# Kernel optimization log

Hardware: AMD Instinct MI355X
Metric: run time of the kernel (lower is better)

## Reference

```python
import jax, jax.numpy as jnp
import numpy as np

SIGMA = 1.5
KSIZE = 15

def _log_kernel(sigma=SIGMA, k=KSIZE):
    ax = np.arange(k, dtype=np.float32) - k // 2
    xx, yy, zz = np.meshgrid(ax, ax, ax, indexing='ij')
    rr2 = xx**2 + yy**2 + zz**2
    g = np.exp(-rr2 / (2.0 * sigma**2))
    g = g / g.sum()
    log = (rr2 - 3.0 * sigma**2) / sigma**4 * g
    log = log - log.mean()
    return jnp.asarray(log.reshape(1, 1, k, k, k), dtype=jnp.float32)  # OIDHW

_KERNEL = _log_kernel()
_PAD = KSIZE // 2

def setup_inputs() -> dict:
    key = jax.random.key(0)
    k1, k2 = jax.random.split(key)
    shape = (4, 160, 160, 160)
    pred = jax.random.normal(k1, shape, dtype=jnp.float32)
    target = jax.random.normal(k2, shape, dtype=jnp.float32)
    return {"pred": pred, "target": target}

def _conv_log(x):
    # x: [B, D, H, W] -> [B, 1, D, H, W] conv with LoG kernel, 'same' padding
    x = x[:, None]  # NCDHW
    return jax.lax.conv_general_dilated(
        x, _KERNEL.astype(x.dtype),
        window_strides=(1, 1, 1),
        padding=[(_PAD, _PAD)] * 3,
        dimension_numbers=('NCDHW', 'OIDHW', 'NCDHW'))

def reference(pred, target):
    fp = _conv_log(pred)
    ft = _conv_log(target)
    return jnp.mean(jnp.abs(fp - ft))
```

## Files before the change

### kernel.cpp

```cpp
#include <hip/hip_runtime.h>
#include <hip/hip_fp16.h>
#include <math.h>

#define KS   15
#define RAD  7
#define L    160
#define VOL  (L*L*L)
#define NB   4
#define WTL  32
#define HTL  80
#define HALO (HTL + 2*RAD)
#define LDA  34
#define RPT  5
#define DT   40
#define NBLK (5*10*16)

typedef float fx2 __attribute__((ext_vector_type(2)));
typedef float fx4 __attribute__((ext_vector_type(4)));

struct Taps {
    float g[KS];
    float h[KS];
    float m;
    float scale;
};

__device__ __forceinline__ fx4 ld4z(const float* __restrict__ p, int w) {
    if (w >= 0 && w + 3 < L) return *reinterpret_cast<const fx4*>(p + w);
    fx4 r;
    r.x = (w     >= 0 && w     < L) ? p[w]     : 0.f;
    r.y = (w + 1 >= 0 && w + 1 < L) ? p[w + 1] : 0.f;
    r.z = (w + 2 >= 0 && w + 2 < L) ? p[w + 2] : 0.f;
    r.w = (w + 3 >= 0 && w + 3 < L) ? p[w + 3] : 0.f;
    return r;
}

__global__ __launch_bounds__(256, 4) void k_wh(const float* __restrict__ pred,
                                               const float* __restrict__ tgt,
                                               __half2* __restrict__ PQ,
                                               __half* __restrict__ Rb,
                                               Taps tp) {
    __shared__ float   sA[HALO][LDA];
    __shared__ float   sB[HALO][LDA];
    __shared__ __half2 sC[HALO][LDA / 2];

    const int pflat = blockIdx.x + 10 * (blockIdx.y + 160 * blockIdx.z);
    const int wlog  = (pflat & 7) * 800 + (pflat >> 3);
    const int bxs   = wlog % 10;
    const int bys   = (wlog / 10) % 160;
    const int bzs   = wlog / 1600;

    const int tid = threadIdx.x;
    const int wt  = bxs >> 1;
    const int ht  = bxs & 1;
    const int wb  = wt * WTL;
    const int h0  = ht * HTL;
    const int d   = bys;
    const int n   = bzs;
    const size_t nbase = (size_t)n * VOL;
    const float* __restrict__ pro = pred + nbase + (size_t)d * L * L;
    const float* __restrict__ tro = tgt  + nbase + (size_t)d * L * L;
    const bool wedge = (wt == 0) || (wt == 4);

    for (int task = tid; task < HALO * 4; task += 256) {
        const int r  = task >> 2;
        const int j2 = task & 3;
        const int h  = h0 - RAD + r;
        if (h >= 0 && h < L) {
            const float* pr = pro + h * L;
            const float* tr = tro + h * L;
            const int w0 = wb + 8 * j2 - 8;
            float dv[24];
            if (!wedge) {
#pragma unroll
                for (int q = 0; q < 6; ++q) {
                    fx4 pv = *reinterpret_cast<const fx4*>(pr + w0 + 4 * q);
                    fx4 tv = *reinterpret_cast<const fx4*>(tr + w0 + 4 * q);
                    fx4 dd = pv - tv;
                    dv[4*q+0] = dd.x; dv[4*q+1] = dd.y;
                    dv[4*q+2] = dd.z; dv[4*q+3] = dd.w;
                }
            } else {
#pragma unroll
                for (int q = 0; q < 6; ++q) {
                    fx4 pv = ld4z(pr, w0 + 4 * q);
                    fx4 tv = ld4z(tr, w0 + 4 * q);
                    fx4 dd = pv - tv;
                    dv[4*q+0] = dd.x; dv[4*q+1] = dd.y;
                    dv[4*q+2] = dd.z; dv[4*q+3] = dd.w;
                }
            }
#pragma unroll
            for (int kp = 0; kp < 8; kp += 2) {
                fx2 mid = {dv[kp + 8], dv[kp + 9]};
                fx2 aa = tp.g[7] * mid;
                fx2 bb = tp.h[7] * mid;
                fx2 cc = mid;
#pragma unroll
                for (int u = 0; u < 7; ++u) {
                    fx2 sl = {dv[kp + 1 + u],  dv[kp + 2 + u]};
                    fx2 sr = {dv[kp + 15 - u], dv[kp + 16 - u]};
                    fx2 s  = sl + sr;
                    aa += tp.g[u] * s;
                    bb += tp.h[u] * s;
                    cc += s;
                }
                *reinterpret_cast<fx2*>(&sA[r][8*j2 + kp]) = aa;
                *reinterpret_cast<fx2*>(&sB[r][8*j2 + kp]) = bb;
                sC[r][(8*j2 + kp) >> 1] = __floats2half2_rn(cc.x, cc.y);
            }
        } else {
#pragma unroll
            for (int kp = 0; kp < 8; kp += 2) {
                fx2 z = {0.f, 0.f};
                *reinterpret_cast<fx2*>(&sA[r][8*j2 + kp]) = z;
                *reinterpret_cast<fx2*>(&sB[r][8*j2 + kp]) = z;
                sC[r][(8*j2 + kp) >> 1] = __floats2half2_rn(0.f, 0.f);
            }
        }
    }
    __syncthreads();

    {
        const int wg = tid & 15;
        const int ty = tid >> 4;
        fx2 p[RPT], q[RPT], rb[RPT];
#pragma unroll
        for (int k = 0; k < RPT; ++k) { p[k] = 0.f; q[k] = 0.f; rb[k] = 0.f; }
#pragma unroll
        for (int jr = 0; jr < RPT + 2 * RAD; ++jr) {
            const int srow = RPT * ty + jr;
            fx2 va = *reinterpret_cast<const fx2*>(&sA[srow][2*wg]);
            fx2 vb = *reinterpret_cast<const fx2*>(&sB[srow][2*wg]);
            float2 cf = __half22float2(sC[srow][wg]);
            fx2 vc = {cf.x, cf.y};
#pragma unroll
            for (int k = 0; k < RPT; ++k) {
                const int t = jr - k;
                if (t >= 0 && t < KS) {
                    p[k]  += tp.g[t] * va;
                    q[k]  += tp.h[t] * va + tp.g[t] * vb;
                    rb[k] += vc;
                }
            }
        }
#pragma unroll
        for (int k = 0; k < RPT; ++k) {
            const int h = h0 + RPT * ty + k;
            const size_t o = nbase + ((size_t)h * L + d) * L + wb + 2*wg;
            __half2 pq[2];
            pq[0] = __floats2half2_rn(p[k].x, q[k].x);
            pq[1] = __floats2half2_rn(p[k].y, q[k].y);
            *reinterpret_cast<int2*>(&PQ[o]) = *reinterpret_cast<int2*>(pq);
            __half2 rr = __floats2half2_rn(rb[k].x, rb[k].y);
            *reinterpret_cast<__half2*>(&Rb[o]) = rr;
        }
    }
}

__global__ __launch_bounds__(512) void k_d(const __half2* __restrict__ PQ,
                                           const __half* __restrict__ R,
                                           float* __restrict__ partial,
                                           Taps tp) {
    const int pflat = blockIdx.x + 5 * (blockIdx.y + 10 * blockIdx.z);
    const int wlog  = (pflat & 7) * 100 + (pflat >> 3);
    const int dc    = wlog & 3;
    const int rest  = wlog >> 2;
    const int bx    = rest % 5;
    const int by    = (rest / 5) % 10;
    const int n     = rest / 50;

    const int tx = threadIdx.x;
    const int ty = threadIdx.y;
    const int w  = bx * 32 + tx;
    const int h  = by * 16 + ty;
    const int d0 = dc * DT;

    const size_t base = (size_t)n * VOL + ((size_t)h * L) * L + w;
    const __half2* PQp = PQ + base;
    const __half*  Rp  = R  + base;

    float rp[KS], rq[KS], rc[KS];
    float box = 0.f;

#pragma unroll
    for (int i = 0; i < KS - 1; ++i) {
        int s = d0 - RAD + i;
        bool ok = (s >= 0);
        int off = s * L;
        float2 pq = make_float2(0.f, 0.f);
        float vc = 0.f;
        if (ok) {
            pq = __half22float2(PQp[off]);
            vc = __half2float(Rp[off]);
        }
        rp[i] = pq.x; rq[i] = pq.y; rc[i] = vc;
        box += vc;
    }

    float acc = 0.f;
#pragma unroll
    for (int k = 0; k < DT; ++k) {
        int s = d0 + RAD + k;
        bool ok = (s < L);
        int off = s * L;
        float2 pq = make_float2(0.f, 0.f);
        float vc = 0.f;
        if (ok) {
            pq = __half22float2(PQp[off]);
            vc = __half2float(Rp[off]);
        }
        const int ri = (KS - 1 + k) % KS;
        rp[ri] = pq.x; rq[ri] = pq.y; rc[ri] = vc;
        box += vc;

        float f = 0.f;
#pragma unroll
        for (int t = 0; t < KS; ++t) {
            const int ii = (k + t) % KS;
            f += tp.h[t] * rp[ii] + tp.g[t] * rq[ii];
        }
        f -= tp.m * box;
        acc += fabsf(f);

        box -= rc[k % KS];
    }
    acc *= tp.scale;

#pragma unroll
    for (int off = 32; off > 0; off >>= 1) acc += __shfl_down(acc, off);

    __shared__ float wsum[8];
    const int tid  = ty * 32 + tx;
    const int lane = tid & 63;
    const int wid  = tid >> 6;
    if (lane == 0) wsum[wid] = acc;
    __syncthreads();
    if (wid == 0) {
        float v = (lane < 8) ? wsum[lane] : 0.f;
#pragma unroll
        for (int off = 4; off > 0; off >>= 1) v += __shfl_down(v, off);
        if (lane == 0) {
            partial[wlog] = v;
        }
    }
}

__global__ __launch_bounds__(1024) void k_reduce(const float* __restrict__ partial,
                                                 float* __restrict__ out) {
    float v = 0.f;
    for (int i = threadIdx.x; i < NBLK; i += 1024) v += partial[i];
#pragma unroll
    for (int off = 32; off > 0; off >>= 1) v += __shfl_down(v, off);

    __shared__ float wsum[16];
    const int lane = threadIdx.x & 63;
    const int wid  = threadIdx.x >> 6;
    if (lane == 0) wsum[wid] = v;
    __syncthreads();
    if (wid == 0) {
        float s = (lane < 16) ? wsum[lane] : 0.f;
#pragma unroll
        for (int off = 8; off > 0; off >>= 1) s += __shfl_down(s, off);
        if (lane == 0) out[0] = s;
    }
}

extern "C" void kernel_launch(void* const* d_in, const int* in_sizes, int n_in,
                              void* d_out, int out_size, void* d_ws, size_t ws_size,
                              hipStream_t stream) {
    const float* pred = (const float*)d_in[0];
    const float* tgt  = (const float*)d_in[1];
    float* out = (float*)d_out;

    Taps tp;
    const double sigma = 1.5;
    double g1[KS], S = 0.0;
    for (int i = 0; i < KS; ++i) {
        double x = (double)(i - RAD);
        g1[i] = exp(-x * x / (2.0 * sigma * sigma));
        S += g1[i];
    }
    double sumH = 0.0;
    for (int i = 0; i < KS; ++i) {
        double x = (double)(i - RAD);
        double G = g1[i] / S;
        double H = (x * x - sigma * sigma) / (sigma * sigma * sigma * sigma) * G;
        tp.g[i] = (float)G;
        tp.h[i] = (float)H;
        sumH += H;
    }
    tp.m     = (float)(3.0 * sumH / (double)(KS * KS * KS));
    tp.scale = 1.0f / ((float)NB * (float)VOL);

    char* wsb = (char*)d_ws;
    __half2* PQ      = (__half2*)wsb;
    __half*  Rb      = (__half*)(wsb + (size_t)NB * VOL * 4);
    float*   partial = (float*)(wsb + (size_t)NB * VOL * 6);

    k_wh<<<dim3(10, L, NB), dim3(256), 0, stream>>>(pred, tgt, PQ, Rb, tp);
    k_d<<<dim3(5, 10, NB * 4), dim3(32, 16), 0, stream>>>(PQ, Rb, partial, tp);
    k_reduce<<<1, 1024, 0, stream>>>(partial, out);
}
```

Measured before the change: 113.3 us.

## Loop k_wh over depth chunks with double-buffered smem and register prefetch

Each k_wh block now handles 10 consecutive depth slices instead of one, ping-ponging two shared-memory buffers. The global loads for the next slice are issued into registers before the current slice's H-pass, and its W-pass runs afterwards, hiding load latency behind compute. Each of 188 threads now does a 16-wide W-conv instead of 8-wide, and zero halo rows are written once. The grid shrinks from 6400 to 640 blocks and occupancy hint drops to 2 per SIMD, which raises register pressure and reduces parallelism.

Result: slower. 149.0 us (+31.4%).

```diff
diff --git a/kernel.cpp b/kernel.cpp
--- a/kernel.cpp
+++ b/kernel.cpp
@@ -12,6 +12,8 @@
 #define HALO (HTL + 2*RAD)
 #define LDA  34
 #define RPT  5
+#define DCH  10
+#define NDC  16
 #define DT   40
 #define NBLK (5*10*16)
 
@@ -35,126 +37,168 @@
     return r;
 }
 
-__global__ __launch_bounds__(256, 4) void k_wh(const float* __restrict__ pred,
+__device__ __forceinline__ void wconv16(const float* dv, const Taps& tp,
+                                        float (*A)[LDA], float (*B)[LDA],
+                                        __half2 (*C)[LDA / 2], int r, int c0) {
+#pragma unroll
+    for (int kp = 0; kp < 16; kp += 2) {
+        fx2 mid = {dv[kp + 8], dv[kp + 9]};
+        fx2 aa = tp.g[7] * mid;
+        fx2 bb = tp.h[7] * mid;
+        fx2 cc = mid;
+#pragma unroll
+        for (int u = 0; u < 7; ++u) {
+            fx2 sl = {dv[kp + 1 + u],  dv[kp + 2 + u]};
+            fx2 sr = {dv[kp + 15 - u], dv[kp + 16 - u]};
+            fx2 s  = sl + sr;
+            aa += tp.g[u] * s;
+            bb += tp.h[u] * s;
+            cc += s;
+        }
+        *reinterpret_cast<fx2*>(&A[r][c0 + kp]) = aa;
+        *reinterpret_cast<fx2*>(&B[r][c0 + kp]) = bb;
+        C[r][(c0 + kp) >> 1] = __floats2half2_rn(cc.x, cc.y);
+    }
+}
+
+__global__ __launch_bounds__(256, 2) void k_wh(const float* __restrict__ pred,
                                                const float* __restrict__ tgt,
                                                __half2* __restrict__ PQ,
                                                __half* __restrict__ Rb,
                                                Taps tp) {
-    __shared__ float   sA[HALO][LDA];
-    __shared__ float   sB[HALO][LDA];
-    __shared__ __half2 sC[HALO][LDA / 2];
-
-    const int pflat = blockIdx.x + 10 * (blockIdx.y + 160 * blockIdx.z);
-    const int wlog  = (pflat & 7) * 800 + (pflat >> 3);
+    __shared__ float   sA[2][HALO][LDA];
+    __shared__ float   sB[2][HALO][LDA];
+    __shared__ __half2 sC[2][HALO][LDA / 2];
+
+    const int pflat = blockIdx.x + 10 * (blockIdx.y + NDC * blockIdx.z);
+    const int wlog  = (pflat & 7) * 80 + (pflat >> 3);
     const int bxs   = wlog % 10;
-    const int bys   = (wlog / 10) % 160;
-    const int bzs   = wlog / 1600;
+    const int dcs   = (wlog / 10) % NDC;
+    const int ns    = wlog / (10 * NDC);
 
     const int tid = threadIdx.x;
     const int wt  = bxs >> 1;
     const int ht  = bxs & 1;
     const int wb  = wt * WTL;
     const int h0  = ht * HTL;
-    const int d   = bys;
-    const int n   = bzs;
+    const int d0  = dcs * DCH;
+    const int n   = ns;
     const size_t nbase = (size_t)n * VOL;
-    const float* __restrict__ pro = pred + nbase + (size_t)d * L * L;
-    const float* __restrict__ tro = tgt  + nbase + (size_t)d * L * L;
     const bool wedge = (wt == 0) || (wt == 4);
 
-    for (int task = tid; task < HALO * 4; task += 256) {
-        const int r  = task >> 2;
-        const int j2 = task & 3;
-        const int h  = h0 - RAD + r;
-        if (h >= 0 && h < L) {
-            const float* pr = pro + h * L;
-            const float* tr = tro + h * L;
-            const int w0 = wb + 8 * j2 - 8;
-            float dv[24];
+    const bool aact = tid < HALO * 2;
+    const int ar  = tid >> 1;
+    const int jh  = tid & 1;
+    const int hh  = h0 - RAD + ar;
+    const bool hok = aact && (hh >= 0) && (hh < L);
+    const int w0 = wb + 16 * jh - 8;
+    const int c0 = 16 * jh;
+
+    const int wg = tid & 15;
+    const int ty = tid >> 4;
+
+    for (int z = tid; z < 7 * LDA; z += 256) {
+        const int zr = z / LDA, zc = z % LDA;
+        const int rr = (ht == 0) ? zr : (HALO - 7 + zr);
+        sA[0][rr][zc] = 0.f; sA[1][rr][zc] = 0.f;
+        sB[0][rr][zc] = 0.f; sB[1][rr][zc] = 0.f;
+        if (zc < LDA / 2) {
+            sC[0][rr][zc] = __floats2half2_rn(0.f, 0.f);
+            sC[1][rr][zc] = __floats2half2_rn(0.f, 0.f);
+        }
+    }
+
+    if (hok) {
+        const float* pr = pred + nbase + (size_t)d0 * L * L + (size_t)hh * L;
+        const float* tr = tgt  + nbase + (size_t)d0 * L * L + (size_t)hh * L;
+        float dv[32];
+#pragma unroll
+        for (int q = 0; q < 8; ++q) {
+            fx4 pv = wedge ? ld4z(pr, w0 + 4 * q)
+                           : *reinterpret_cast<const fx4*>(pr + w0 + 4 * q);
+            fx4 tv = wedge ? ld4z(tr, w0 + 4 * q)
+                           : *reinterpret_cast<const fx4*>(tr + w0 + 4 * q);
+            fx4 dd = pv - tv;
+            dv[4*q+0] = dd.x; dv[4*q+1] = dd.y; dv[4*q+2] = dd.z; dv[4*q+3] = dd.w;
+        }
+        wconv16(dv, tp, sA[0], sB[0], sC[0], ar, c0);
+    }
+    __syncthreads();
+
+    int cur = 0;
+    for (int i = 0; i < DCH; ++i) {
+        const int d = d0 + i;
+        const bool pf = (i < DCH - 1) && hok;
+
+        fx4 pv[8], tv[8];
+        if (pf) {
+            const float* pr = pred + nbase + (size_t)(d + 1) * L * L + (size_t)hh * L;
+            const float* tr = tgt  + nbase + (size_t)(d + 1) * L * L + (size_t)hh * L;
             if (!wedge) {
 #pragma unroll
-                for (int q = 0; q < 6; ++q) {
-                    fx4 pv = *reinterpret_cast<const fx4*>(pr + w0 + 4 * q);
-                    fx4 tv = *reinterpret_cast<const fx4*>(tr + w0 + 4 * q);
-                    fx4 dd = pv - tv;
-                    dv[4*q+0] = dd.x; dv[4*q+1] = dd.y;
-                    dv[4*q+2] = dd.z; dv[4*q+3] = dd.w;
+                for (int q = 0; q < 8; ++q) {
+                    pv[q] = *reinterpret_cast<const fx4*>(pr + w0 + 4 * q);
+                    tv[q] = *reinterpret_cast<const fx4*>(tr + w0 + 4 * q);
                 }
             } else {
 #pragma unroll
-                for (int q = 0; q < 6; ++q) {
-                    fx4 pv = ld4z(pr, w0 + 4 * q);
-                    fx4 tv = ld4z(tr, w0 + 4 * q);
-                    fx4 dd = pv - tv;
-                    dv[4*q+0] = dd.x; dv[4*q+1] = dd.y;
-                    dv[4*q+2] = dd.z; dv[4*q+3] = dd.w;
+                for (int q = 0; q < 8; ++q) {
+                    pv[q] = ld4z(pr, w0 + 4 * q);
+                    tv[q] = ld4z(tr, w0 + 4 * q);
                 }
             }
-#pragma unroll
-            for (int kp = 0; kp < 8; kp += 2) {
-                fx2 mid = {dv[kp + 8], dv[kp + 9]};
-                fx2 aa = tp.g[7] * mid;
-                fx2 bb = tp.h[7] * mid;
-                fx2 cc = mid;
-#pragma unroll
-                for (int u = 0; u < 7; ++u) {
-                    fx2 sl = {dv[kp + 1 + u],  dv[kp + 2 + u]};
-                    fx2 sr = {dv[kp + 15 - u], dv[kp + 16 - u]};
-                    fx2 s  = sl + sr;
-                    aa += tp.g[u] * s;
-                    bb += tp.h[u] * s;
-                    cc += s;
-                }
-                *reinterpret_cast<fx2*>(&sA[r][8*j2 + kp]) = aa;
-                *reinterpret_cast<fx2*>(&sB[r][8*j2 + kp]) = bb;
-                sC[r][(8*j2 + kp) >> 1] = __floats2half2_rn(cc.x, cc.y);
-            }
-        } else {
-#pragma unroll
-            for (int kp = 0; kp < 8; kp += 2) {
-                fx2 z = {0.f, 0.f};
-                *reinterpret_cast<fx2*>(&sA[r][8*j2 + kp]) = z;
-                *reinterpret_cast<fx2*>(&sB[r][8*j2 + kp]) = z;
-                sC[r][(8*j2 + kp) >> 1] = __floats2half2_rn(0.f, 0.f);
-            }
-        }
-    }
-    __syncthreads();
-
-    {
-        const int wg = tid & 15;
-        const int ty = tid >> 4;
-        fx2 p[RPT], q[RPT], rb[RPT];
-#pragma unroll
-        for (int k = 0; k < RPT; ++k) { p[k] = 0.f; q[k] = 0.f; rb[k] = 0.f; }
-#pragma unroll
-        for (int jr = 0; jr < RPT + 2 * RAD; ++jr) {
-            const int srow = RPT * ty + jr;
-            fx2 va = *reinterpret_cast<const fx2*>(&sA[srow][2*wg]);
-            fx2 vb = *reinterpret_cast<const fx2*>(&sB[srow][2*wg]);
-            float2 cf = __half22float2(sC[srow][wg]);
-            fx2 vc = {cf.x, cf.y};
-#pragma unroll
-            for (int k = 0; k < RPT; ++k) {
-                const int t = jr - k;
-                if (t >= 0 && t < KS) {
-                    p[k]  += tp.g[t] * va;
-                    q[k]  += tp.h[t] * va + tp.g[t] * vb;
-                    rb[k] += vc;
+        }
+
+        {
+            float (*cA)[LDA]     = sA[cur];
+            float (*cB)[LDA]     = sB[cur];
+            __half2 (*cC)[LDA/2] = sC[cur];
+            fx2 p[RPT], q[RPT], rb[RPT];
+#pragma unroll
+            for (int k = 0; k < RPT; ++k) { p[k] = 0.f; q[k] = 0.f; rb[k] = 0.f; }
+#pragma unroll
+            for (int jr = 0; jr < RPT + 2 * RAD; ++jr) {
+                const int srow = RPT * ty + jr;
+                fx2 va = *reinterpret_cast<const fx2*>(&cA[srow][2 * wg]);
+                fx2 vb = *reinterpret_cast<const fx2*>(&cB[srow][2 * wg]);
+                float2 cf = __half22float2(cC[srow][wg]);
+                fx2 vc = {cf.x, cf.y};
+#pragma unroll
+                for (int k = 0; k < RPT; ++k) {
+                    const int t = jr - k;
+                    if (t >= 0 && t < KS) {
+                        p[k]  += tp.g[t] * va;
+                        q[k]  += tp.h[t] * va + tp.g[t] * vb;
+                        rb[k] += vc;
+                    }
                 }
             }
-        }
-#pragma unroll
-        for (int k = 0; k < RPT; ++k) {
-            const int h = h0 + RPT * ty + k;
-            const size_t o = nbase + ((size_t)h * L + d) * L + wb + 2*wg;
-            __half2 pq[2];
-            pq[0] = __floats2half2_rn(p[k].x, q[k].x);
-            pq[1] = __floats2half2_rn(p[k].y, q[k].y);
-            *reinterpret_cast<int2*>(&PQ[o]) = *reinterpret_cast<int2*>(pq);
-            __half2 rr = __floats2half2_rn(rb[k].x, rb[k].y);
-            *reinterpret_cast<__half2*>(&Rb[o]) = rr;
-        }
+#pragma unroll
+            for (int k = 0; k < RPT; ++k) {
+                const int h = h0 + RPT * ty + k;
+                const size_t o = nbase + ((size_t)h * L + d) * L + wb + 2 * wg;
+                __half2 pq[2];
+                pq[0] = __floats2half2_rn(p[k].x, q[k].x);
+                pq[1] = __floats2half2_rn(p[k].y, q[k].y);
+                *reinterpret_cast<int2*>(&PQ[o]) = *reinterpret_cast<int2*>(pq);
+                __half2 rr = __floats2half2_rn(rb[k].x, rb[k].y);
+                *reinterpret_cast<__half2*>(&Rb[o]) = rr;
+            }
+        }
+
+        if (pf) {
+            float dv[32];
+#pragma unroll
+            for (int q8 = 0; q8 < 8; ++q8) {
+                fx4 dd = pv[q8] - tv[q8];
+                dv[4*q8+0] = dd.x; dv[4*q8+1] = dd.y;
+                dv[4*q8+2] = dd.z; dv[4*q8+3] = dd.w;
+            }
+            wconv16(dv, tp, sA[cur ^ 1], sB[cur ^ 1], sC[cur ^ 1], ar, c0);
+        }
+
+        if (i < DCH - 1) __syncthreads();
+        cur ^= 1;
     }
 }
 
@@ -298,7 +342,7 @@
     __half*  Rb      = (__half*)(wsb + (size_t)NB * VOL * 4);
     float*   partial = (float*)(wsb + (size_t)NB * VOL * 6);
 
-    k_wh<<<dim3(10, L, NB), dim3(256), 0, stream>>>(pred, tgt, PQ, Rb, tp);
+    k_wh<<<dim3(10, NDC, NB), dim3(256), 0, stream>>>(pred, tgt, PQ, Rb, tp);
     k_d<<<dim3(5, 10, NB * 4), dim3(32, 16), 0, stream>>>(PQ, Rb, partial, tp);
     k_reduce<<<1, 1024, 0, stream>>>(partial, out);
 }
```
